# Kernel optimization log

Hardware: AMD Instinct MI355X
Metric: run time of the kernel (lower is better)

## Reference

```python
import jax, jax.numpy as jnp
import numpy as np

N = 2048          # recurrent units (args_dict['n'])
B = 128           # batch
T = 1024          # timesteps
INHIB_PROP = 0.2  # args_dict['inhib_proportion']
SAT_LO, SAT_HI = 0.0, 1.0e8  # saturations -> effectively ReLU


def setup_inputs() -> dict:
    key = jax.random.key(0)
    ks = jax.random.split(key, 8)
    std = 1.0 / np.sqrt(N)
    x0 = jax.random.normal(ks[0], (B, T), jnp.float32)
    x1 = jax.random.normal(ks[1], (B, T), jnp.float32)
    enc0 = jax.random.normal(ks[2], (N,), jnp.float32) * std
    enc1 = jax.random.normal(ks[3], (N,), jnp.float32) * std
    dec0 = jax.random.normal(ks[4], (N,), jnp.float32) * std
    dec1 = jax.random.normal(ks[5], (N,), jnp.float32) * std
    # Dale constraint: W must be elementwise non-negative (asserted in integrate).
    # Scale 1/N keeps the effective spectral radius < 1 for a stable recurrence.
    W = jax.random.uniform(ks[6], (N, N), jnp.float32) * (1.0 / N)
    n_inhib = int(N * INHIB_PROP)
    signs = jnp.concatenate([jnp.ones(N - n_inhib, jnp.float32),
                             -jnp.ones(n_inhib, jnp.float32)])
    mask = jnp.ones((N,), jnp.float32)
    state0 = jnp.zeros((N,), jnp.float32)
    return {"x0": x0, "x1": x1, "enc0": enc0, "enc1": enc1,
            "dec0": dec0, "dec1": dec1, "W": W, "signs": signs,
            "mask": mask, "state0": state0}


def reference(x0, x1, enc0, enc1, dec0, dec1, W, signs, mask, state0):
    # Effective recurrent matrix: W @ diag(signs); state update uses its transpose.
    Weff_T = (W * signs[None, :]).T  # [N, N]

    def step(state, xt):  # state: [B, N]
        i0, i1 = xt  # each [B]
        ext = enc0[None, :] * i0[:, None] + enc1[None, :] * i1[:, None]  # [B, N]
        new_state = mask * jnp.clip((state + mask * ext) @ Weff_T, SAT_LO, SAT_HI)
        o0 = (dec0 * new_state).sum(-1)  # [B]
        o1 = (dec1 * new_state).sum(-1)  # [B]
        return new_state, (o0, o1)

    init = jnp.broadcast_to(state0, (x0.shape[0], state0.shape[0]))  # [B, N]
    _, (o0, o1) = jax.lax.scan(step, init, (x0.T, x1.T))  # outputs [T, B]
    return o0.T, o1.T  # each [B, T]
```

## Files before the change

kernel.cpp:

```cpp
#include <hip/hip_runtime.h>
#include <hip/hip_bf16.h>
#include <stdint.h>


#define NN 2048
#define BB 128
#define TT 1024

typedef __attribute__((ext_vector_type(8)))  __bf16          bf16x8;
typedef __attribute__((ext_vector_type(8)))  unsigned short  ushort8;
typedef __attribute__((ext_vector_type(16))) float           f32x16;

#define IF_OFF   0u
#define IF_FRAGS 32768
#define CTR_OFF  (1u << 20)
#define CTR_BYTES 2048u

__device__ __forceinline__ unsigned short f2bf(float f) {
    __hip_bfloat16 h = __float2bfloat16(f);
    return *reinterpret_cast<unsigned short*>(&h);
}

__global__ void init_pack(const float* __restrict__ x0, const float* __restrict__ x1,
                          const float* __restrict__ enc0, const float* __restrict__ enc1,
                          const float* __restrict__ mask, const float* __restrict__ state0,
                          unsigned short* __restrict__ If)
{
    int idx  = blockIdx.x * 256 + threadIdx.x;
    int e    = idx & 7;
    int lane = (idx >> 3) & 63;
    int kt   = (idx >> 9) & 127;
    int p    = idx >> 16;
    int b    = p * 32 + (lane & 31);
    int j    = kt * 16 + ((lane >> 5) << 3) + e;
    float v  = state0[j] + mask[j] * (enc0[j] * x0[(size_t)b * TT]
                                    + enc1[j] * x1[(size_t)b * TT]);
    If[idx] = f2bf(v);
}

#define LDS_TOTAL 153856

__global__ void __launch_bounds__(512, 2)
dale_persistent(const float* __restrict__ x0, const float* __restrict__ x1,
                const float* __restrict__ enc0, const float* __restrict__ enc1,
                const float* __restrict__ dec0, const float* __restrict__ dec1,
                const float* __restrict__ W, const float* __restrict__ signs,
                const float* __restrict__ mask,
                unsigned short* __restrict__ If,
                unsigned int* __restrict__ ctr,
                float* __restrict__ out)
{
    extern __shared__ char lds[];
    float* red   = reinterpret_cast<float*>(lds + 131072);
    float* nsbuf = reinterpret_cast<float*>(lds + 131072 + 17408);
    float* ldsC  = reinterpret_cast<float*>(lds + 131072 + 17408 + 4352);
    float* xbuf  = reinterpret_cast<float*>(lds + 131072 + 17408 + 4352 + 768);

    const int tid  = threadIdx.x;
    const int wave = tid >> 6;
    const int lane = tid & 63;
    const int wg   = blockIdx.x;
    const int p  = (wg & 7) >> 1;
    const int q  = ((wg & 1) << 5) | (wg >> 3);
    const int b0 = p * 32;
    const int i0 = q * 32;

    for (int o = tid; o < 8192; o += 512) {
        int il8 = o >> 8;
        int k8  = o & 255;
        const float* wr = W + (size_t)(i0 + il8) * NN + k8 * 8;
        const float* sg = signs + k8 * 8;
        ushort8 pk;
        #pragma unroll
        for (int e = 0; e < 8; ++e) pk[e] = f2bf(wr[e] * sg[e]);
        int slot = k8 ^ il8;
        *reinterpret_cast<ushort8*>(lds + il8 * 4096 + slot * 16) = pk;
    }
    if (tid < 32) {
        ldsC[tid]       = mask[i0 + tid];
        ldsC[32 + tid]  = dec0[i0 + tid];
        ldsC[64 + tid]  = dec1[i0 + tid];
        ldsC[96 + tid]  = enc0[i0 + tid];
        ldsC[128 + tid] = enc1[i0 + tid];
    }
    __syncthreads();

    const int il = lane & 31;
    const int hi = lane >> 5;
    char* wrow = lds + il * 4096;

    const bf16x8* ApBase = reinterpret_cast<const bf16x8*>(If)
                         + (p * 128 + wave * 16) * 64 + lane;
    unsigned int* waitCtr = ctr + ((p * 8 + wave) << 4);
    unsigned int* arrCtr  = ctr + ((p * 8 + (q >> 3)) << 4);

    const float mk  = ldsC[il];
    const float e0c = ldsC[96 + il];
    const float e1c = ldsC[128 + il];
    const int jl   = i0 + il;
    const int kt_l = jl >> 4;
    const int hb_l = (jl >> 3) & 1;
    const int e_l  = jl & 7;
    unsigned short* sb0 = If + ((size_t)(p * 128 + kt_l) * 64) * 8 + e_l + hb_l * 256;
    unsigned short* sb1 = sb0 + (size_t)IF_FRAGS * 8;

    const int eb = tid >> 4;
    const int ei = (tid & 15) * 2;
    const float d00 = ldsC[32 + ei], d01 = ldsC[32 + ei + 1];
    const float d10 = ldsC[64 + ei], d11 = ldsC[64 + ei + 1];
    float* out0 = out + (size_t)(b0 + eb) * TT;
    float* out1 = out + (size_t)BB * TT + (size_t)(b0 + eb) * TT;

    for (int t = 0; t < TT; ++t) {
        const int par = t & 1;

        if (t > 0) {
            const unsigned tgt = 16u * (unsigned)t;
            int guard = 0;
            for (;;) {
                unsigned vv = 0;
                if (lane == 0)
                    vv = __hip_atomic_load(waitCtr, __ATOMIC_RELAXED,
                                           __HIP_MEMORY_SCOPE_AGENT);
                unsigned v = (unsigned)__shfl((int)vv, 0, 64);
                if (v >= tgt || ++guard >= (1 << 17)) break;
                __builtin_amdgcn_s_sleep(1);
            }
        }

        if (wave == 0) {
            int bb = lane & 31;
            const float* xs = (lane < 32) ? x0 : x1;
            float v = (t + 1 < TT) ? xs[(size_t)(b0 + bb) * TT + (t + 1)] : 0.f;
            xbuf[hi * 32 + bb] = v;
        }

        bf16x8 A[16];
        const bf16x8* ap = ApBase + (size_t)par * IF_FRAGS;
        #pragma unroll
        for (int it = 0; it < 16; ++it) {
            const bf16x8* aptr = ap + it * 64;
            asm volatile("global_load_dwordx4 %0, %1, off sc0 sc1"
                         : "=v"(A[it]) : "v"(aptr) : "memory");
        }

        f32x16 acc;
        #pragma unroll
        for (int r = 0; r < 16; ++r) acc[r] = 0.f;

        asm volatile("s_waitcnt vmcnt(8)" ::: "memory");
        __builtin_amdgcn_sched_barrier(0);
        #pragma unroll
        for (int it = 0; it < 8; ++it) {
            int kt   = wave * 16 + it;
            int slot = (kt * 2 + hi) ^ il;
            bf16x8 b = *reinterpret_cast<const bf16x8*>(wrow + slot * 16);
            acc = __builtin_amdgcn_mfma_f32_32x32x16_bf16(A[it], b, acc, 0, 0, 0);
        }
        asm volatile("s_waitcnt vmcnt(0)" ::: "memory");
        __builtin_amdgcn_sched_barrier(0);
        #pragma unroll
        for (int it = 8; it < 16; ++it) {
            int kt   = wave * 16 + it;
            int slot = (kt * 2 + hi) ^ il;
            bf16x8 b = *reinterpret_cast<const bf16x8*>(wrow + slot * 16);
            acc = __builtin_amdgcn_mfma_f32_32x32x16_bf16(A[it], b, acc, 0, 0, 0);
        }

        if (wave >= 4) {
            float* d = red + (wave - 4) * 1088 + lane * 17;
            #pragma unroll
            for (int r = 0; r < 16; ++r) d[r] = acc[r];
        }
        __syncthreads();
        if (wave < 4) {
            const float* s = red + wave * 1088 + lane * 17;
            #pragma unroll
            for (int r = 0; r < 16; ++r) acc[r] += s[r];
            if (wave >= 2) {
                float* d = red + wave * 1088 + lane * 17;
                #pragma unroll
                for (int r = 0; r < 16; ++r) d[r] = acc[r];
            }
        }
        __syncthreads();
        if (wave == 0) {
            const float* s = red + 2 * 1088 + lane * 17;
            #pragma unroll
            for (int r = 0; r < 16; ++r) acc[r] += s[r];
            float* d = red + lane * 17;
            #pragma unroll
            for (int rr = 0; rr < 8; ++rr) d[rr] = acc[8 + rr];
        } else if (wave == 1) {
            const float* s = red + 3 * 1088 + lane * 17;
            #pragma unroll
            for (int r = 0; r < 16; ++r) acc[r] += s[r];
            float* d = red + 1088 + lane * 17;
            #pragma unroll
            for (int rr = 0; rr < 8; ++rr) d[rr] = acc[rr];
        }
        __syncthreads();

        if (wave < 2) {
            const float* s = red + (1 ^ wave) * 1088 + lane * 17;
            unsigned short* sb = (par == 0) ? sb1 : sb0;
            #pragma unroll
            for (int rr = 0; rr < 8; ++rr) {
                int   r    = (wave << 3) + rr;
                float raw  = acc[r] + s[rr];
                int   brow = (r & 3) + 8 * (r >> 2) + 4 * hi;
                float ns   = fminf(fmaxf(raw, 0.f), 1e8f) * mk;
                nsbuf[brow * 34 + il] = ns;
                if (t + 1 < TT) {
                    float v = ns + mk * (e0c * xbuf[brow] + e1c * xbuf[32 + brow]);
                    unsigned int pv = (unsigned int)f2bf(v);
                    const unsigned short* dst = sb + brow * 8;
                    asm volatile("global_store_short %0, %1, off sc0 sc1"
                                 :: "v"(dst), "v"(pv) : "memory");
                }
            }
            if (t + 1 < TT) {
                asm volatile("s_waitcnt vmcnt(0)" ::: "memory");
                if (lane == 0)
                    __hip_atomic_fetch_add(arrCtr, 1u, __ATOMIC_RELAXED,
                                           __HIP_MEMORY_SCOPE_AGENT);
            }
        }
        __syncthreads();

        {
            float ns0 = nsbuf[eb * 34 + ei];
            float ns1 = nsbuf[eb * 34 + ei + 1];
            float o0p = d00 * ns0 + d01 * ns1;
            float o1p = d10 * ns0 + d11 * ns1;
            #pragma unroll
            for (int m = 8; m >= 1; m >>= 1) {
                o0p += __shfl_xor(o0p, m);
                o1p += __shfl_xor(o1p, m);
            }
            if ((tid & 15) == 0) {
                atomicAdd(out0 + t, o0p);
                atomicAdd(out1 + t, o1p);
            }
        }
    }
}

extern "C" void kernel_launch(void* const* d_in, const int* in_sizes, int n_in,
                              void* d_out, int out_size, void* d_ws, size_t ws_size,
                              hipStream_t stream)
{
    (void)in_sizes; (void)n_in; (void)ws_size;
    const float* x0    = (const float*)d_in[0];
    const float* x1    = (const float*)d_in[1];
    const float* enc0  = (const float*)d_in[2];
    const float* enc1  = (const float*)d_in[3];
    const float* dec0  = (const float*)d_in[4];
    const float* dec1  = (const float*)d_in[5];
    const float* W     = (const float*)d_in[6];
    const float* signs = (const float*)d_in[7];
    const float* mask  = (const float*)d_in[8];
    const float* st0   = (const float*)d_in[9];

    unsigned short* If  = (unsigned short*)((char*)d_ws + IF_OFF);
    unsigned int*   ctr = (unsigned int*)((char*)d_ws + CTR_OFF);
    float*          out = (float*)d_out;

    hipMemsetAsync(d_out, 0, sizeof(float) * (size_t)out_size, stream);
    hipMemsetAsync(ctr, 0, CTR_BYTES, stream);

    init_pack<<<1024, 256, 0, stream>>>(x0, x1, enc0, enc1, mask, st0, If);

    hipFuncSetAttribute(reinterpret_cast<const void*>(&dale_persistent),
                        hipFuncAttributeMaxDynamicSharedMemorySize, LDS_TOTAL);
    dale_persistent<<<256, 512, LDS_TOTAL, stream>>>(
        x0, x1, enc0, enc1, dec0, dec1, W, signs, mask, If, ctr, out);
}
```

Before: 6.979 ms.

## Halve workgroup count by giving each block 64 output columns, half of W in registers

Each persistent workgroup now computes 64 output units instead of 32, with the second 32-row W slice held in VGPRs as bf16 fragments while the first stays in LDS. The grid shrinks from 256 to 128 blocks, so each block reuses its loaded A fragments for two MFMA chains and fewer blocks take part in the per-step counter barrier (arrival target drops from 16 to 4). The cost is much higher register pressure, a second serialized cross-wave reduction with extra __syncthreads per step, and half as many CUs doing the per-step math.

```diff
diff --git a/kernel.cpp b/kernel.cpp
--- a/kernel.cpp
+++ b/kernel.cpp
@@ -20,6 +20,8 @@
     __hip_bfloat16 h = __float2bfloat16(f);
     return *reinterpret_cast<unsigned short*>(&h);
 }
+
+union CV8 { ushort8 u; bf16x8 b; };
 
 __global__ void init_pack(const float* __restrict__ x0, const float* __restrict__ x1,
                           const float* __restrict__ enc0, const float* __restrict__ enc1,
@@ -38,7 +40,7 @@
     If[idx] = f2bf(v);
 }
 
-#define LDS_TOTAL 153856
+#define LDS_TOTAL 158464
 
 __global__ void __launch_bounds__(512, 2)
 dale_persistent(const float* __restrict__ x0, const float* __restrict__ x1,
@@ -52,18 +54,37 @@
 {
     extern __shared__ char lds[];
     float* red   = reinterpret_cast<float*>(lds + 131072);
-    float* nsbuf = reinterpret_cast<float*>(lds + 131072 + 17408);
-    float* ldsC  = reinterpret_cast<float*>(lds + 131072 + 17408 + 4352);
-    float* xbuf  = reinterpret_cast<float*>(lds + 131072 + 17408 + 4352 + 768);
+    float* nsbuf = reinterpret_cast<float*>(lds + 148480);
+    float* ldsC  = reinterpret_cast<float*>(lds + 156928);
+    float* xbuf  = reinterpret_cast<float*>(lds + 158208);
 
     const int tid  = threadIdx.x;
     const int wave = tid >> 6;
     const int lane = tid & 63;
     const int wg   = blockIdx.x;
-    const int p  = (wg & 7) >> 1;
-    const int q  = ((wg & 1) << 5) | (wg >> 3);
+    const int p  = wg & 3;
+    const int q  = wg >> 2;
     const int b0 = p * 32;
-    const int i0 = q * 32;
+    const int i0 = q * 64;
+
+    const int il = lane & 31;
+    const int hi = lane >> 5;
+
+    bf16x8 breg[16];
+    {
+        const int row = i0 + 32 + il;
+        const float* wrow_g = W + (size_t)row * NN;
+        #pragma unroll
+        for (int it = 0; it < 16; ++it) {
+            int kb = (wave * 16 + it) * 16 + hi * 8;
+            const float* wr = wrow_g + kb;
+            const float* sg = signs + kb;
+            CV8 cv;
+            #pragma unroll
+            for (int e = 0; e < 8; ++e) cv.u[e] = f2bf(wr[e] * sg[e]);
+            breg[it] = cv.b;
+        }
+    }
 
     for (int o = tid; o < 8192; o += 512) {
         int il8 = o >> 8;
@@ -76,38 +97,37 @@
         int slot = k8 ^ il8;
         *reinterpret_cast<ushort8*>(lds + il8 * 4096 + slot * 16) = pk;
     }
-    if (tid < 32) {
-        ldsC[tid]       = mask[i0 + tid];
-        ldsC[32 + tid]  = dec0[i0 + tid];
-        ldsC[64 + tid]  = dec1[i0 + tid];
-        ldsC[96 + tid]  = enc0[i0 + tid];
-        ldsC[128 + tid] = enc1[i0 + tid];
+    if (tid < 64) {
+        ldsC[tid]        = mask[i0 + tid];
+        ldsC[64 + tid]   = dec0[i0 + tid];
+        ldsC[128 + tid]  = dec1[i0 + tid];
+        ldsC[192 + tid]  = enc0[i0 + tid];
+        ldsC[256 + tid]  = enc1[i0 + tid];
     }
     __syncthreads();
 
-    const int il = lane & 31;
-    const int hi = lane >> 5;
     char* wrow = lds + il * 4096;
 
     const bf16x8* ApBase = reinterpret_cast<const bf16x8*>(If)
                          + (p * 128 + wave * 16) * 64 + lane;
     unsigned int* waitCtr = ctr + ((p * 8 + wave) << 4);
-    unsigned int* arrCtr  = ctr + ((p * 8 + (q >> 3)) << 4);
-
-    const float mk  = ldsC[il];
-    const float e0c = ldsC[96 + il];
-    const float e1c = ldsC[128 + il];
-    const int jl   = i0 + il;
-    const int kt_l = jl >> 4;
-    const int hb_l = (jl >> 3) & 1;
-    const int e_l  = jl & 7;
-    unsigned short* sb0 = If + ((size_t)(p * 128 + kt_l) * 64) * 8 + e_l + hb_l * 256;
-    unsigned short* sb1 = sb0 + (size_t)IF_FRAGS * 8;
+    unsigned int* arrCtr  = ctr + ((p * 8 + (q >> 2)) << 4);
+
+    const float mkA  = ldsC[il],        mkB  = ldsC[32 + il];
+    const float e0A  = ldsC[192 + il],  e0B  = ldsC[224 + il];
+    const float e1A  = ldsC[256 + il],  e1B  = ldsC[288 + il];
+    const int jA = i0 + il, jB = i0 + 32 + il;
+    unsigned short* sbA = If + ((size_t)(p * 128 + (jA >> 4)) * 64) * 8
+                        + (jA & 7) + ((jA >> 3) & 1) * 256;
+    unsigned short* sbB = If + ((size_t)(p * 128 + (jB >> 4)) * 64) * 8
+                        + (jB & 7) + ((jB >> 3) & 1) * 256;
 
     const int eb = tid >> 4;
-    const int ei = (tid & 15) * 2;
-    const float d00 = ldsC[32 + ei], d01 = ldsC[32 + ei + 1];
-    const float d10 = ldsC[64 + ei], d11 = ldsC[64 + ei + 1];
+    const int ec = (tid & 15) * 4;
+    const float d00 = ldsC[64 + ec],  d01 = ldsC[64 + ec + 1];
+    const float d02 = ldsC[64 + ec + 2], d03 = ldsC[64 + ec + 3];
+    const float d10 = ldsC[128 + ec], d11 = ldsC[128 + ec + 1];
+    const float d12 = ldsC[128 + ec + 2], d13 = ldsC[128 + ec + 3];
     float* out0 = out + (size_t)(b0 + eb) * TT;
     float* out1 = out + (size_t)BB * TT + (size_t)(b0 + eb) * TT;
 
@@ -115,7 +135,7 @@
         const int par = t & 1;
 
         if (t > 0) {
-            const unsigned tgt = 16u * (unsigned)t;
+            const unsigned tgt = 4u * (unsigned)t;
             int guard = 0;
             for (;;) {
                 unsigned vv = 0;
@@ -128,7 +148,7 @@
             }
         }
 
-        if (wave == 0) {
+        if (wave == 7) {
             int bb = lane & 31;
             const float* xs = (lane < 32) ? x0 : x1;
             float v = (t + 1 < TT) ? xs[(size_t)(b0 + bb) * TT + (t + 1)] : 0.f;
@@ -144,9 +164,9 @@
                          : "=v"(A[it]) : "v"(aptr) : "memory");
         }
 
-        f32x16 acc;
-        #pragma unroll
-        for (int r = 0; r < 16; ++r) acc[r] = 0.f;
+        f32x16 acc0, acc1;
+        #pragma unroll
+        for (int r = 0; r < 16; ++r) { acc0[r] = 0.f; acc1[r] = 0.f; }
 
         asm volatile("s_waitcnt vmcnt(8)" ::: "memory");
         __builtin_amdgcn_sched_barrier(0);
@@ -154,8 +174,9 @@
         for (int it = 0; it < 8; ++it) {
             int kt   = wave * 16 + it;
             int slot = (kt * 2 + hi) ^ il;
-            bf16x8 b = *reinterpret_cast<const bf16x8*>(wrow + slot * 16);
-            acc = __builtin_amdgcn_mfma_f32_32x32x16_bf16(A[it], b, acc, 0, 0, 0);
+            bf16x8 bl = *reinterpret_cast<const bf16x8*>(wrow + slot * 16);
+            acc0 = __builtin_amdgcn_mfma_f32_32x32x16_bf16(A[it], bl, acc0, 0, 0, 0);
+            acc1 = __builtin_amdgcn_mfma_f32_32x32x16_bf16(A[it], breg[it], acc1, 0, 0, 0);
         }
         asm volatile("s_waitcnt vmcnt(0)" ::: "memory");
         __builtin_amdgcn_sched_barrier(0);
@@ -163,62 +184,104 @@
         for (int it = 8; it < 16; ++it) {
             int kt   = wave * 16 + it;
             int slot = (kt * 2 + hi) ^ il;
-            bf16x8 b = *reinterpret_cast<const bf16x8*>(wrow + slot * 16);
-            acc = __builtin_amdgcn_mfma_f32_32x32x16_bf16(A[it], b, acc, 0, 0, 0);
+            bf16x8 bl = *reinterpret_cast<const bf16x8*>(wrow + slot * 16);
+            acc0 = __builtin_amdgcn_mfma_f32_32x32x16_bf16(A[it], bl, acc0, 0, 0, 0);
+            acc1 = __builtin_amdgcn_mfma_f32_32x32x16_bf16(A[it], breg[it], acc1, 0, 0, 0);
         }
 
         if (wave >= 4) {
             float* d = red + (wave - 4) * 1088 + lane * 17;
             #pragma unroll
-            for (int r = 0; r < 16; ++r) d[r] = acc[r];
+            for (int r = 0; r < 16; ++r) d[r] = acc0[r];
         }
         __syncthreads();
         if (wave < 4) {
             const float* s = red + wave * 1088 + lane * 17;
             #pragma unroll
-            for (int r = 0; r < 16; ++r) acc[r] += s[r];
+            for (int r = 0; r < 16; ++r) acc0[r] += s[r];
             if (wave >= 2) {
                 float* d = red + wave * 1088 + lane * 17;
                 #pragma unroll
-                for (int r = 0; r < 16; ++r) d[r] = acc[r];
+                for (int r = 0; r < 16; ++r) d[r] = acc0[r];
             }
         }
         __syncthreads();
         if (wave == 0) {
             const float* s = red + 2 * 1088 + lane * 17;
             #pragma unroll
-            for (int r = 0; r < 16; ++r) acc[r] += s[r];
-            float* d = red + lane * 17;
-            #pragma unroll
-            for (int rr = 0; rr < 8; ++rr) d[rr] = acc[8 + rr];
+            for (int r = 0; r < 16; ++r) acc0[r] += s[r];
         } else if (wave == 1) {
             const float* s = red + 3 * 1088 + lane * 17;
-            #pragma unroll
-            for (int r = 0; r < 16; ++r) acc[r] += s[r];
             float* d = red + 1088 + lane * 17;
             #pragma unroll
-            for (int rr = 0; rr < 8; ++rr) d[rr] = acc[rr];
-        }
-        __syncthreads();
-
-        if (wave < 2) {
-            const float* s = red + (1 ^ wave) * 1088 + lane * 17;
-            unsigned short* sb = (par == 0) ? sb1 : sb0;
-            #pragma unroll
-            for (int rr = 0; rr < 8; ++rr) {
-                int   r    = (wave << 3) + rr;
-                float raw  = acc[r] + s[rr];
+            for (int r = 0; r < 16; ++r) { acc0[r] += s[r]; d[r] = acc0[r]; }
+        }
+        __syncthreads();
+        if (wave == 0) {
+            const float* s = red + 1088 + lane * 17;
+            unsigned short* sb = sbA + ((par == 0) ? (size_t)IF_FRAGS * 8 : 0);
+            #pragma unroll
+            for (int r = 0; r < 16; ++r) {
+                float raw  = acc0[r] + s[r];
                 int   brow = (r & 3) + 8 * (r >> 2) + 4 * hi;
-                float ns   = fminf(fmaxf(raw, 0.f), 1e8f) * mk;
-                nsbuf[brow * 34 + il] = ns;
+                float ns   = fminf(fmaxf(raw, 0.f), 1e8f) * mkA;
+                nsbuf[brow * 66 + il] = ns;
                 if (t + 1 < TT) {
-                    float v = ns + mk * (e0c * xbuf[brow] + e1c * xbuf[32 + brow]);
+                    float v = ns + mkA * (e0A * xbuf[brow] + e1A * xbuf[32 + brow]);
                     unsigned int pv = (unsigned int)f2bf(v);
                     const unsigned short* dst = sb + brow * 8;
                     asm volatile("global_store_short %0, %1, off sc0 sc1"
                                  :: "v"(dst), "v"(pv) : "memory");
                 }
             }
+        }
+        __syncthreads();
+
+        if (wave >= 4) {
+            float* d = red + (wave - 4) * 1088 + lane * 17;
+            #pragma unroll
+            for (int r = 0; r < 16; ++r) d[r] = acc1[r];
+        }
+        __syncthreads();
+        if (wave < 4) {
+            const float* s = red + wave * 1088 + lane * 17;
+            #pragma unroll
+            for (int r = 0; r < 16; ++r) acc1[r] += s[r];
+            if (wave >= 2) {
+                float* d = red + wave * 1088 + lane * 17;
+                #pragma unroll
+                for (int r = 0; r < 16; ++r) d[r] = acc1[r];
+            }
+        }
+        __syncthreads();
+        if (wave == 0) {
+            const float* s = red + 2 * 1088 + lane * 17;
+            #pragma unroll
+            for (int r = 0; r < 16; ++r) acc1[r] += s[r];
+        } else if (wave == 1) {
+            const float* s = red + 3 * 1088 + lane * 17;
+            float* d = red + 1088 + lane * 17;
+            #pragma unroll
+            for (int r = 0; r < 16; ++r) { acc1[r] += s[r]; d[r] = acc1[r]; }
+        }
+        __syncthreads();
+        if (wave == 0) {
+            const float* s = red + 1088 + lane * 17;
+            unsigned short* sb = sbB + ((par == 0) ? (size_t)IF_FRAGS * 8 : 0);
+            #pragma unroll
+            for (int r = 0; r < 16; ++r) {
+                float raw  = acc1[r] + s[r];
+                int   brow = (r & 3) + 8 * (r >> 2) + 4 * hi;
+                float ns   = fminf(fmaxf(raw, 0.f), 1e8f) * mkB;
+                nsbuf[brow * 66 + 32 + il] = ns;
+                if (t + 1 < TT) {
+                    float v = ns + mkB * (e0B * xbuf[brow] + e1B * xbuf[32 + brow]);
+                    unsigned int pv = (unsigned int)f2bf(v);
+                    const unsigned short* dst = sb + brow * 8;
+                    asm volatile("global_store_short %0, %1, off sc0 sc1"
+                                 :: "v"(dst), "v"(pv) : "memory");
+                }
+            }
             if (t + 1 < TT) {
                 asm volatile("s_waitcnt vmcnt(0)" ::: "memory");
                 if (lane == 0)
@@ -229,10 +292,10 @@
         __syncthreads();
 
         {
-            float ns0 = nsbuf[eb * 34 + ei];
-            float ns1 = nsbuf[eb * 34 + ei + 1];
-            float o0p = d00 * ns0 + d01 * ns1;
-            float o1p = d10 * ns0 + d11 * ns1;
+            const float* nsr = nsbuf + eb * 66 + ec;
+            float n0 = nsr[0], n1 = nsr[1], n2 = nsr[2], n3 = nsr[3];
+            float o0p = d00 * n0 + d01 * n1 + d02 * n2 + d03 * n3;
+            float o1p = d10 * n0 + d11 * n1 + d12 * n2 + d13 * n3;
             #pragma unroll
             for (int m = 8; m >= 1; m >>= 1) {
                 o0p += __shfl_xor(o0p, m);
@@ -273,6 +336,6 @@
 
     hipFuncSetAttribute(reinterpret_cast<const void*>(&dale_persistent),
                         hipFuncAttributeMaxDynamicSharedMemorySize, LDS_TOTAL);
-    dale_persistent<<<256, 512, LDS_TOTAL, stream>>>(
+    dale_persistent<<<128, 512, LDS_TOTAL, stream>>>(
         x0, x1, enc0, enc1, dec0, dec1, W, signs, mask, If, ctr, out);
 }
```

New measurement: 9.327 ms. 33.7% more time.
